# Kernel tuning notes

Hardware: AMD Instinct MI355X
Metric: run time of the kernel (lower is better)

Reference implementation:

```python
import jax, jax.numpy as jnp
import numpy as np

EPS = 1e-3  # eps in grad_pursuit_update_step


def _grad_pursuit(signal, dictionary, target_l0):
    """signal: [B, V], dictionary: [F, V] -> dense weights [B, F] (nonneg)."""
    B, V = signal.shape
    F = dictionary.shape[0]
    rows = jnp.arange(B)

    def step(weights, _):
        # residual = signal - weights @ D         [B, V]
        residual = signal - jnp.einsum('bf,fv->bv', weights, dictionary)
        # inner products with every atom          [B, F]
        inner = jnp.einsum('bv,fv->bf', residual, dictionary)
        idx = jnp.argmax(inner, axis=1)           # [B]
        selected = (weights != 0).at[rows, idx].set(True)
        grad = jnp.where(selected, inner, jnp.zeros((), signal.dtype))  # [B, F]
        c = jnp.einsum('bf,fv->bv', grad, dictionary)                   # [B, V]
        c_sq = jnp.sum(c * c, axis=-1)
        step_size = jnp.sum(c * residual, axis=-1) / jnp.maximum(c_sq, EPS)
        weights = jax.nn.relu(weights + step_size[:, None] * grad)
        return weights, None

    w0 = jnp.zeros((B, F), dtype=signal.dtype)
    weights, _ = jax.lax.scan(step, w0, None, length=target_l0)
    return weights


def _decode(indices, weights, dictionary):
    # embedding-bag sum: gather rows then weighted sum over k
    return jnp.einsum('bk,bkv->bv', weights, dictionary[indices])


def setup_inputs() -> dict:
    key = jax.random.key(0)
    k1, k2, k3, k4, k5 = jax.random.split(key, 5)
    B, D, F = 1024, 1024, 8192
    x = jax.random.normal(k1, (B, D), dtype=jnp.float32)
    y = jax.random.normal(k2, (B, D), dtype=jnp.float32)
    xs = jax.random.normal(k3, (F, D), dtype=jnp.float32)
    xs = xs / jnp.linalg.norm(xs, axis=-1, keepdims=True)  # module stores unit-norm atoms
    ys = jax.random.normal(k4, (F, D), dtype=jnp.float32)
    ys = ys / jnp.linalg.norm(jax.random.normal(k3, (F, D)), axis=-1, keepdims=True)
    mean_y = 0.1 * jax.random.normal(k5, (D,), dtype=jnp.float32)
    return {"x": x, "y": y, "xs": xs, "ys": ys, "mean_y": mean_y, "target_l0": 16}


def reference(x, y, xs, ys, mean_y, target_l0):
    # ITDA.forward with subtract_mean=False, skip_connection=False, fvu_loss=True
    dense = _grad_pursuit(x, xs, target_l0)               # [B, F]
    weights, indices = jax.lax.top_k(dense, target_l0)    # [B, k], [B, k]
    x_rec = _decode(indices, weights, xs)                  # [B, V]
    y_rec = _decode(indices, weights, ys)                  # [B, V]
    l2 = jnp.sum((y - y_rec) ** 2, axis=-1)                # [B]
    total_var = jnp.mean(jnp.sum((y - mean_y) ** 2, axis=-1))
    losses = l2 / total_var
    return weights, indices, x_rec, y_rec, losses
```

## Files before the change

### kernel.cpp

```cpp
#include <hip/hip_runtime.h>
#include <cstdint>
#include <cstddef>

#define B_N 1024
#define V_N 1024
#define F_N 8192
#define NSEL 16
#define NITER 16
#define EPSV 1e-3f
#define WINF 0.008f
#define CANDMAX 64
#define NTILE 64

#define BM 64
#define BN 128
#define BK 32
#define NBN (F_N / BN)

typedef __attribute__((ext_vector_type(4))) float f32x4;
typedef __attribute__((ext_vector_type(8))) short bf16x8;
typedef unsigned short u16;

#define GLDS16(g, l) __builtin_amdgcn_global_load_lds((__attribute__((address_space(1))) void*)(g), (__attribute__((address_space(3))) void*)(l), 16, 0, 0)

__device__ __forceinline__ u16 f2bf(float f) {
  unsigned u = __float_as_uint(f);
  return (u16)((u + 0x7FFFu + ((u >> 16) & 1u)) >> 16);
}

__device__ __forceinline__ float block_sum256(float v, float* sbuf) {
#pragma unroll
  for (int o = 32; o > 0; o >>= 1) v += __shfl_down(v, o, 64);
  int lane = threadIdx.x & 63, wid = threadIdx.x >> 6;
  if (lane == 0) sbuf[wid] = v;
  __syncthreads();
  float r = sbuf[0] + sbuf[1] + sbuf[2] + sbuf[3];
  __syncthreads();
  return r;
}

__device__ __forceinline__ float block_max256(float v, float* sbuf) {
#pragma unroll
  for (int o = 32; o > 0; o >>= 1) v = fmaxf(v, __shfl_down(v, o, 64));
  int lane = threadIdx.x & 63, wid = threadIdx.x >> 6;
  if (lane == 0) sbuf[wid] = v;
  __syncthreads();
  float r = fmaxf(fmaxf(sbuf[0], sbuf[1]), fmaxf(sbuf[2], sbuf[3]));
  __syncthreads();
  return r;
}

__device__ __forceinline__ float seq_dot(const float* __restrict__ xrow,
                                         const float* __restrict__ sr) {
  float acc = 0.f;
  for (int k = 0; k < V_N; k += 4) {
    float4 xv = *(const float4*)(xrow + k);
    acc = __builtin_fmaf(xv.x, sr[k + 0], acc);
    acc = __builtin_fmaf(xv.y, sr[k + 1], acc);
    acc = __builtin_fmaf(xv.z, sr[k + 2], acc);
    acc = __builtin_fmaf(xv.w, sr[k + 3], acc);
  }
  return acc;
}

__global__ __launch_bounds__(256) void rowvar_kernel(const float* __restrict__ y,
                                                     const float* __restrict__ mean_y,
                                                     float* __restrict__ rowvar,
                                                     int* __restrict__ act_cnt) {
  int b = blockIdx.x, t = threadIdx.x;
  __shared__ float sred[4];
  float4 yv = *(const float4*)(y + (size_t)b * V_N + t * 4);
  float4 mv = *(const float4*)(mean_y + t * 4);
  float dx = yv.x - mv.x, dy = yv.y - mv.y, dz = yv.z - mv.z, dw = yv.w - mv.w;
  float p = dx * dx + dy * dy + dz * dz + dw * dw;
  float s = block_sum256(p, sred);
  if (t == 0) { rowvar[b] = s; act_cnt[b] = 0; }
}

__global__ __launch_bounds__(256) void reduce_var_kernel(const float* __restrict__ rowvar,
                                                         float* __restrict__ totvar) {
  __shared__ float sred[4];
  int t = threadIdx.x;
  float p = 0.f;
#pragma unroll
  for (int i = 0; i < 4; i++) p += rowvar[t * 4 + i];
  float s = block_sum256(p, sred);
  if (t == 0) totvar[0] = s / (float)B_N;
}

__global__ __launch_bounds__(256) void xh_kernel(const float* __restrict__ xs,
                                                 u16* __restrict__ Xh) {
  int b = blockIdx.x, t = threadIdx.x;
  float4 v = *(const float4*)(xs + (size_t)b * V_N + t * 4);
  u16* o = Xh + (size_t)b * V_N + t * 4;
  o[0] = f2bf(v.x); o[1] = f2bf(v.y); o[2] = f2bf(v.z); o[3] = f2bf(v.w);
}

__global__ __launch_bounds__(256) void init_kernel(const float* __restrict__ x,
                                                   float* __restrict__ R,
                                                   u16* __restrict__ Rh,
                                                   float* __restrict__ rn2) {
  int b = blockIdx.x, t = threadIdx.x;
  __shared__ float sred[4];
  float4 v = *(const float4*)(x + (size_t)b * V_N + t * 4);
  *(float4*)(R + (size_t)b * V_N + t * 4) = v;
  u16* o = Rh + (size_t)b * V_N + t * 4;
  o[0] = f2bf(v.x); o[1] = f2bf(v.y); o[2] = f2bf(v.z); o[3] = f2bf(v.w);
  float p = v.x * v.x + v.y * v.y + v.z * v.z + v.w * v.w;
  float s = block_sum256(p, sred);
  if (t == 0) rn2[b] = s;
}

__global__ __launch_bounds__(256) void gemm_scan_kernel(const u16* __restrict__ Rh,
                                                        const u16* __restrict__ Xh,
                                                        float* __restrict__ inner,
                                                        float* __restrict__ pval) {
  __shared__ u16 As[128 * 32];
  __shared__ u16 Bs[128 * 32];
  __shared__ float srmax[128][2];
  const int tid = threadIdx.x;
  const int w = tid >> 6, l = tid & 63;
  const int bn = blockIdx.x, bm = blockIdx.y;
  const int wr = w >> 1, wc = w & 1;
  const int lr = l & 15, lg = l >> 4;

  f32x4 acc[4][4];
#pragma unroll
  for (int m = 0; m < 4; m++)
#pragma unroll
    for (int n = 0; n < 4; n++) acc[m][n] = (f32x4){0.f, 0.f, 0.f, 0.f};

  const u16* Ab = Rh + (size_t)bm * 128 * V_N;
  const u16* Bb = Xh + (size_t)bn * 128 * V_N;
  const int srow = w * 16 + (l >> 2);
  const int scol = (l & 3) * 8;

  for (int k0 = 0; k0 < V_N; k0 += 32) {
#pragma unroll
    for (int i = 0; i < 2; i++) {
      GLDS16(Ab + (size_t)(i * 64 + srow) * V_N + k0 + scol, As + i * 2048 + w * 512);
      GLDS16(Bb + (size_t)(i * 64 + srow) * V_N + k0 + scol, Bs + i * 2048 + w * 512);
    }
    __syncthreads();
    bf16x8 af[4], bfr[4];
#pragma unroll
    for (int m = 0; m < 4; m++) af[m] = *(const bf16x8*)&As[(wr * 64 + m * 16 + lr) * 32 + lg * 8];
#pragma unroll
    for (int n = 0; n < 4; n++) bfr[n] = *(const bf16x8*)&Bs[(wc * 64 + n * 16 + lr) * 32 + lg * 8];
#pragma unroll
    for (int m = 0; m < 4; m++)
#pragma unroll
      for (int n = 0; n < 4; n++)
        acc[m][n] = __builtin_amdgcn_mfma_f32_16x16x32_bf16(af[m], bfr[n], acc[m][n], 0, 0, 0);
    __syncthreads();
  }

#pragma unroll
  for (int m = 0; m < 4; m++) {
    int gm = bm * 128 + wr * 64 + m * 16 + lg * 4;
#pragma unroll
    for (int j = 0; j < 4; j++) {
      float pm = acc[m][0][j];
#pragma unroll
      for (int n = 1; n < 4; n++) pm = fmaxf(pm, acc[m][n][j]);
#pragma unroll
      for (int n = 0; n < 4; n++) {
        int gn = bn * 128 + wc * 64 + n * 16 + lr;
        inner[(size_t)(gm + j) * F_N + gn] = acc[m][n][j];
      }
#pragma unroll
      for (int mk = 1; mk < 16; mk <<= 1) pm = fmaxf(pm, __shfl_xor(pm, mk, 64));
      if (lr == 0) srmax[wr * 64 + m * 16 + lg * 4 + j][wc] = pm;
    }
  }
  __syncthreads();
  if (tid < 128) {
    float v = fmaxf(srmax[tid][0], srmax[tid][1]);
    pval[(size_t)(bm * 128 + tid) * NTILE + bn] = v;
  }
}

__global__ __launch_bounds__(256) void scan_update_kernel(const float* __restrict__ x,
                                                          const float* __restrict__ xs,
                                                          const float* __restrict__ inner,
                                                          const float* __restrict__ pval,
                                                          float* __restrict__ rn2,
                                                          int* __restrict__ act_ids,
                                                          float* __restrict__ act_w,
                                                          int* __restrict__ act_cnt,
                                                          float* __restrict__ R,
                                                          u16* __restrict__ Rh) {
  int b = blockIdx.x, t = threadIdx.x;
  __shared__ float sr[V_N];
  __shared__ float spv[NTILE];
  __shared__ int   shot[NTILE];
  __shared__ int   snhot;
  __shared__ float sred[4];
  __shared__ float smax[4];
  __shared__ int   scand[CANDMAX];
  __shared__ float scval[CANDMAX];
  __shared__ float sfv[256];
  __shared__ int   sfi[256];
  __shared__ int   scnt_c;
  __shared__ int   sbii;
  __shared__ float sg[NSEL + 2];
  __shared__ float sw[NSEL + 2];
  __shared__ int   sids[NSEL + 2];
  __shared__ int   ssel[NSEL + 2];
  __shared__ int   scnt;

  float4 rv = *(const float4*)(R + (size_t)b * V_N + t * 4);
  *(float4*)&sr[t * 4] = rv;
  if (t < NTILE) spv[t] = pval[(size_t)b * NTILE + t];
  if (t == 0) { scnt_c = 0; snhot = 0; }
  __syncthreads();

  float M = block_max256(spv[t & (NTILE - 1)], smax);
  float win = WINF * sqrtf(rn2[b]);
  float thr = M - win;

  if (t < NTILE && spv[t] >= thr) { int p = atomicAdd(&snhot, 1); shot[p] = t; }
  __syncthreads();
  int nh = snhot;

  const float* irow = inner + (size_t)b * F_N;
  for (int h = 0; h < nh; h++) {
    int tt = shot[h];
    if (t < 128) {
      float v = irow[tt * 128 + t];
      if (v >= thr) { int p = atomicAdd(&scnt_c, 1); if (p < CANDMAX) scand[p] = tt * 128 + t; }
    }
  }
  __syncthreads();
  int total = scnt_c;
  int nc = total < CANDMAX ? total : CANDMAX;

  if (total > CANDMAX) {
    float bv = -1e30f; int bi = 0x7fffffff;
    for (int f = t; f < F_N; f += 256) {
      float acc = seq_dot(xs + (size_t)f * V_N, sr);
      if (acc > bv) { bv = acc; bi = f; }
    }
    sfv[t] = bv; sfi[t] = bi;
    __syncthreads();
    if (t == 0) {
      float bbv = sfv[0]; int bbi = sfi[0];
      for (int c = 1; c < 256; c++) {
        float v = sfv[c]; int id = sfi[c];
        if (v > bbv || (v == bbv && id < bbi)) { bbv = v; bbi = id; }
      }
      sbii = bbi;
    }
  } else if (nc == 1) {
    if (t == 0) sbii = scand[0];
  } else {
    if (t < nc) scval[t] = seq_dot(xs + (size_t)scand[t] * V_N, sr);
    __syncthreads();
    if (t == 0) {
      float bv = scval[0]; int bi = scand[0];
      for (int c = 1; c < nc; c++) {
        float v = scval[c]; int id = scand[c];
        if (v > bv || (v == bv && id < bi)) { bv = v; bi = id; }
      }
      sbii = bi;
    }
  }
  __syncthreads();

  if (t == 0) {
    int bi = sbii;
    int cnt = act_cnt[b];
    for (int j = 0; j < cnt; j++) { sids[j] = act_ids[b * NSEL + j]; sw[j] = act_w[b * NSEL + j]; }
    int pos = -1;
    for (int j = 0; j < cnt; j++) if (sids[j] == bi) pos = j;
    if (pos < 0) { pos = cnt; sids[cnt] = bi; sw[cnt] = 0.f; cnt++; }
    for (int j = 0; j < cnt; j++) ssel[j] = (sw[j] != 0.f) || (j == pos) ? 1 : 0;
    scnt = cnt;
  }
  __syncthreads();
  int cnt = scnt;

  float4 rl = *(const float4*)&sr[t * 4];
  float4 xv[NSEL + 1];
#pragma unroll
  for (int j = 0; j < NSEL + 1; j++) {
    if (j < cnt) {
      if (ssel[j]) {
        xv[j] = *(const float4*)(xs + (size_t)sids[j] * V_N + t * 4);
        float p = xv[j].x * rl.x + xv[j].y * rl.y + xv[j].z * rl.z + xv[j].w * rl.w;
        float s = block_sum256(p, sred);
        if (t == 0) sg[j] = s;
      } else if (t == 0) sg[j] = 0.f;
    }
  }
  __syncthreads();

  float4 cv = {0.f, 0.f, 0.f, 0.f};
#pragma unroll
  for (int j = 0; j < NSEL + 1; j++) {
    if (j < cnt) {
      if (ssel[j]) {
        float g = sg[j];
        cv.x += g * xv[j].x; cv.y += g * xv[j].y; cv.z += g * xv[j].z; cv.w += g * xv[j].w;
      }
    }
  }
  float pcsq = cv.x * cv.x + cv.y * cv.y + cv.z * cv.z + cv.w * cv.w;
  float pcr  = cv.x * rl.x + cv.y * rl.y + cv.z * rl.z + cv.w * rl.w;
  float csq = block_sum256(pcsq, sred);
  float cr  = block_sum256(pcr, sred);

  if (t == 0) {
    float step = cr / fmaxf(csq, EPSV);
    for (int j = 0; j < cnt; j++)
      if (ssel[j]) sw[j] = fmaxf(sw[j] + step * sg[j], 0.f);
    for (int j = 0; j < cnt; j++) {
      act_ids[b * NSEL + j] = sids[j];
      act_w[b * NSEL + j] = sw[j];
    }
    act_cnt[b] = cnt;
  }
  __syncthreads();

  float4 r = *(const float4*)(x + (size_t)b * V_N + t * 4);
#pragma unroll
  for (int j = 0; j < NSEL + 1; j++) {
    if (j < cnt) {
      float wv = sw[j];
      if (wv != 0.f) {
        r.x -= wv * xv[j].x; r.y -= wv * xv[j].y; r.z -= wv * xv[j].z; r.w -= wv * xv[j].w;
      }
    }
  }
  *(float4*)(R + (size_t)b * V_N + t * 4) = r;
  u16* o = Rh + (size_t)b * V_N + t * 4;
  o[0] = f2bf(r.x); o[1] = f2bf(r.y); o[2] = f2bf(r.z); o[3] = f2bf(r.w);
  float p2 = r.x * r.x + r.y * r.y + r.z * r.z + r.w * r.w;
  float s2 = block_sum256(p2, sred);
  if (t == 0) rn2[b] = s2;
}

__global__ __launch_bounds__(256) void residual_kernel(const float* __restrict__ x,
                                                       const float* __restrict__ xs,
                                                       const int* __restrict__ act_ids,
                                                       const float* __restrict__ act_w,
                                                       const int* __restrict__ act_cnt,
                                                       float* __restrict__ R) {
  int b = blockIdx.x, t = threadIdx.x;
  float4 r = *(const float4*)(x + (size_t)b * V_N + t * 4);
  int cnt = act_cnt[b];
  for (int j = 0; j < cnt; j++) {
    float w = act_w[b * NSEL + j];
    if (w != 0.f) {
      const float* xr = xs + (size_t)act_ids[b * NSEL + j] * V_N;
      float4 xv = *(const float4*)(xr + t * 4);
      r.x -= w * xv.x; r.y -= w * xv.y; r.z -= w * xv.z; r.w -= w * xv.w;
    }
  }
  *(float4*)(R + (size_t)b * V_N + t * 4) = r;
}

__global__ __launch_bounds__(256) void gemm_argmax_kernel(const float* __restrict__ R,
                                                          const float* __restrict__ xs,
                                                          float* __restrict__ pval,
                                                          int* __restrict__ pidx) {
  __shared__ float sA[BK * 68];
  __shared__ float sB[BK * 132];
  __shared__ float sMv[64 * 33];
  __shared__ int   sMi[64 * 33];

  int tid = threadIdx.x;
  int bn = blockIdx.x, bm = blockIdx.y;
  float acc[8][4];
#pragma unroll
  for (int i = 0; i < 8; i++)
#pragma unroll
    for (int j = 0; j < 4; j++) acc[i][j] = 0.f;

  int r0 = (tid >> 5) << 3;
  int n0 = (tid & 31) << 2;
  const float* Rbase = R + (size_t)(bm * BM) * V_N;
  const float* Xbase = xs + (size_t)(bn * BN) * V_N;

  for (int k0 = 0; k0 < V_N; k0 += BK) {
    {
      int m = tid >> 2, kf = (tid & 3) * 4;
      float4 v = *(const float4*)(Rbase + (size_t)m * V_N + k0 + kf);
      sA[(kf + 0) * 68 + m] = v.x; sA[(kf + 1) * 68 + m] = v.y;
      sA[(kf + 2) * 68 + m] = v.z; sA[(kf + 3) * 68 + m] = v.w;
      float4 v2 = *(const float4*)(Rbase + (size_t)m * V_N + k0 + kf + 16);
      sA[(kf + 16) * 68 + m] = v2.x; sA[(kf + 17) * 68 + m] = v2.y;
      sA[(kf + 18) * 68 + m] = v2.z; sA[(kf + 19) * 68 + m] = v2.w;
    }
    {
      int nn = tid >> 3, kf = (tid & 7) * 4;
#pragma unroll
      for (int i = 0; i < 4; i++) {
        int n = nn + i * 32;
        float4 v = *(const float4*)(Xbase + (size_t)n * V_N + k0 + kf);
        sB[(kf + 0) * 132 + n] = v.x; sB[(kf + 1) * 132 + n] = v.y;
        sB[(kf + 2) * 132 + n] = v.z; sB[(kf + 3) * 132 + n] = v.w;
      }
    }
    __syncthreads();
#pragma unroll
    for (int k = 0; k < BK; k++) {
      float4 aL = *(float4*)&sA[k * 68 + r0];
      float4 aH = *(float4*)&sA[k * 68 + r0 + 4];
      float4 bv = *(float4*)&sB[k * 132 + n0];
      float a[8] = {aL.x, aL.y, aL.z, aL.w, aH.x, aH.y, aH.z, aH.w};
      float bb[4] = {bv.x, bv.y, bv.z, bv.w};
#pragma unroll
      for (int i = 0; i < 8; i++)
#pragma unroll
        for (int j = 0; j < 4; j++) acc[i][j] += a[i] * bb[j];
    }
    __syncthreads();
  }

#pragma unroll
  for (int i = 0; i < 8; i++) {
    float bvv = acc[i][0]; int bj = 0;
#pragma unroll
    for (int j = 1; j < 4; j++)
      if (acc[i][j] > bvv) { bvv = acc[i][j]; bj = j; }
    sMv[(r0 + i) * 33 + (tid & 31)] = bvv;
    sMi[(r0 + i) * 33 + (tid & 31)] = bn * BN + n0 + bj;
  }
  __syncthreads();
  if (tid < 64) {
    float bvv = sMv[tid * 33]; int bi = sMi[tid * 33];
    for (int c = 1; c < 32; c++) {
      float v = sMv[tid * 33 + c];
      if (v > bvv) { bvv = v; bi = sMi[tid * 33 + c]; }
    }
    pval[(size_t)(bm * BM + tid) * NBN + bn] = bvv;
    pidx[(size_t)(bm * BM + tid) * NBN + bn] = bi;
  }
}

__global__ __launch_bounds__(256) void combine_update_kernel(const float* __restrict__ R,
                                                             const float* __restrict__ xs,
                                                             const float* __restrict__ pval,
                                                             const int* __restrict__ pidx,
                                                             int* __restrict__ act_ids,
                                                             float* __restrict__ act_w,
                                                             int* __restrict__ act_cnt) {
  int b = blockIdx.x, t = threadIdx.x;
  __shared__ float sr[V_N];
  __shared__ float sred[4];
  __shared__ float sg[NSEL + 1];
  __shared__ float sw[NSEL + 1];
  __shared__ int   sids[NSEL + 1];
  __shared__ int   ssel[NSEL + 1];
  __shared__ int   scnt;

  float4 rv = *(const float4*)(R + (size_t)b * V_N + t * 4);
  *(float4*)&sr[t * 4] = rv;

  if (t == 0) {
    const float* pv = pval + (size_t)b * NBN;
    const int* pi = pidx + (size_t)b * NBN;
    float bv = pv[0]; int bi = pi[0];
    for (int c = 1; c < NBN; c++) {
      float v = pv[c];
      if (v > bv) { bv = v; bi = pi[c]; }
    }
    int cnt = act_cnt[b];
    for (int j = 0; j < cnt; j++) { sids[j] = act_ids[b * NSEL + j]; sw[j] = act_w[b * NSEL + j]; }
    int pos = -1;
    for (int j = 0; j < cnt; j++) if (sids[j] == bi) pos = j;
    if (pos < 0) { pos = cnt; sids[cnt] = bi; sw[cnt] = 0.f; cnt++; }
    for (int j = 0; j < cnt; j++) ssel[j] = (sw[j] != 0.f) || (j == pos) ? 1 : 0;
    scnt = cnt;
  }
  __syncthreads();
  int cnt = scnt;

  for (int j = 0; j < cnt; j++) {
    if (!ssel[j]) { if (t == 0) sg[j] = 0.f; continue; }
    const float* xr = xs + (size_t)sids[j] * V_N;
    float4 xv = *(const float4*)(xr + t * 4);
    float4 rl = *(const float4*)&sr[t * 4];
    float p = xv.x * rl.x + xv.y * rl.y + xv.z * rl.z + xv.w * rl.w;
    float s = block_sum256(p, sred);
    if (t == 0) sg[j] = s;
  }
  __syncthreads();

  float4 cv = {0.f, 0.f, 0.f, 0.f};
  for (int j = 0; j < cnt; j++) {
    if (ssel[j]) {
      float g = sg[j];
      const float* xr = xs + (size_t)sids[j] * V_N;
      float4 xv = *(const float4*)(xr + t * 4);
      cv.x += g * xv.x; cv.y += g * xv.y; cv.z += g * xv.z; cv.w += g * xv.w;
    }
  }
  float4 rl = *(const float4*)&sr[t * 4];
  float pcsq = cv.x * cv.x + cv.y * cv.y + cv.z * cv.z + cv.w * cv.w;
  float pcr  = cv.x * rl.x + cv.y * rl.y + cv.z * rl.z + cv.w * rl.w;
  float csq = block_sum256(pcsq, sred);
  float cr  = block_sum256(pcr, sred);

  if (t == 0) {
    float step = cr / fmaxf(csq, EPSV);
    for (int j = 0; j < cnt; j++)
      if (ssel[j]) sw[j] = fmaxf(sw[j] + step * sg[j], 0.f);
    for (int j = 0; j < cnt; j++) {
      act_ids[b * NSEL + j] = sids[j];
      act_w[b * NSEL + j] = sw[j];
    }
    act_cnt[b] = cnt;
  }
}

__global__ __launch_bounds__(256) void topk_kernel(const int* __restrict__ act_ids,
                                                   const float* __restrict__ act_w,
                                                   const int* __restrict__ act_cnt,
                                                   float* __restrict__ out_w,
                                                   float* __restrict__ out_i) {
  int b = blockIdx.x * blockDim.x + threadIdx.x;
  if (b >= B_N) return;
  int cnt = act_cnt[b];
  int ids[NSEL]; float w[NSEL]; int m = 0;
  for (int j = 0; j < cnt; j++) {
    float wv = act_w[b * NSEL + j];
    if (wv > 0.f) { ids[m] = act_ids[b * NSEL + j]; w[m] = wv; m++; }
  }
  for (int i = 1; i < m; i++) {
    float wv = w[i]; int id = ids[i]; int j = i - 1;
    while (j >= 0 && (w[j] < wv || (w[j] == wv && ids[j] > id))) {
      w[j + 1] = w[j]; ids[j + 1] = ids[j]; j--;
    }
    w[j + 1] = wv; ids[j + 1] = id;
  }
  int nf = 0;
  for (int s = m; s < NSEL; s++) {
    for (;;) {
      bool used = false;
      for (int j = 0; j < m; j++) if (ids[j] == nf) used = true;
      if (!used) break;
      nf++;
    }
    ids[s] = nf; w[s] = 0.f; nf++;
  }
  for (int s = 0; s < NSEL; s++) {
    out_w[b * NSEL + s] = w[s];
    out_i[b * NSEL + s] = (float)ids[s];
  }
}

__global__ __launch_bounds__(256) void decode_kernel(const float* __restrict__ y,
                                                     const float* __restrict__ xs,
                                                     const float* __restrict__ ys,
                                                     const float* __restrict__ out_w,
                                                     const float* __restrict__ out_i,
                                                     const float* __restrict__ totvar,
                                                     float* __restrict__ x_rec,
                                                     float* __restrict__ y_rec,
                                                     float* __restrict__ losses) {
  int b = blockIdx.x, t = threadIdx.x;
  __shared__ float swv[NSEL];
  __shared__ int sid[NSEL];
  __shared__ float sred[4];
  if (t < NSEL) { swv[t] = out_w[b * NSEL + t]; sid[t] = (int)out_i[b * NSEL + t]; }
  __syncthreads();
  float4 xr = {0.f, 0.f, 0.f, 0.f}, yr = {0.f, 0.f, 0.f, 0.f};
  for (int s = 0; s < NSEL; s++) {
    float wv = swv[s];
    if (wv != 0.f) {
      const float* xrow = xs + (size_t)sid[s] * V_N;
      const float* yrow = ys + (size_t)sid[s] * V_N;
      float4 a = *(const float4*)(xrow + t * 4);
      float4 c = *(const float4*)(yrow + t * 4);
      xr.x += wv * a.x; xr.y += wv * a.y; xr.z += wv * a.z; xr.w += wv * a.w;
      yr.x += wv * c.x; yr.y += wv * c.y; yr.z += wv * c.z; yr.w += wv * c.w;
    }
  }
  *(float4*)(x_rec + (size_t)b * V_N + t * 4) = xr;
  *(float4*)(y_rec + (size_t)b * V_N + t * 4) = yr;
  float4 yv = *(const float4*)(y + (size_t)b * V_N + t * 4);
  float dx = yv.x - yr.x, dy = yv.y - yr.y, dz = yv.z - yr.z, dw = yv.w - yr.w;
  float p = dx * dx + dy * dy + dz * dz + dw * dw;
  float l2 = block_sum256(p, sred);
  if (t == 0) losses[b] = l2 / totvar[0];
}

extern "C" void kernel_launch(void* const* d_in, const int* in_sizes, int n_in,
                              void* d_out, int out_size, void* d_ws, size_t ws_size,
                              hipStream_t stream) {
  const float* x      = (const float*)d_in[0];
  const float* y      = (const float*)d_in[1];
  const float* xs     = (const float*)d_in[2];
  const float* ys     = (const float*)d_in[3];
  const float* mean_y = (const float*)d_in[4];
  (void)in_sizes; (void)n_in; (void)out_size;

  float* out    = (float*)d_out;
  float* out_w  = out;
  float* out_i  = out + 16384;
  float* out_xr = out + 32768;
  float* out_yr = out + 32768 + 1048576;
  float* out_ls = out + 32768 + 2097152;

  float* ws = (float*)d_ws;

  const size_t FAST_NEED = (size_t)14257153 * 4;

  if (ws_size >= FAST_NEED) {
    float* R     = ws;
    float* inner = ws + 1048576;
    u16*   Rh    = (u16*)(ws + 9437184);
    u16*   Xh    = (u16*)(ws + 9961472);
    float* rn2   = ws + 14155776;
    int*   aid   = (int*)(ws + 14156800);
    float* aw    = ws + 14173184;
    int*   acn   = (int*)(ws + 14189568);
    float* rv    = ws + 14190592;
    float* tv    = ws + 14191616;
    float* pval  = ws + 14191617;

    rowvar_kernel<<<B_N, 256, 0, stream>>>(y, mean_y, rv, acn);
    reduce_var_kernel<<<1, 256, 0, stream>>>(rv, tv);
    xh_kernel<<<F_N, 256, 0, stream>>>(xs, Xh);
    init_kernel<<<B_N, 256, 0, stream>>>(x, R, Rh, rn2);

    for (int it = 0; it < NITER; it++) {
      gemm_scan_kernel<<<dim3(F_N / 128, B_N / 128), 256, 0, stream>>>(Rh, Xh, inner, pval);
      scan_update_kernel<<<B_N, 256, 0, stream>>>(x, xs, inner, pval, rn2, aid, aw, acn, R, Rh);
    }

    topk_kernel<<<(B_N + 255) / 256, 256, 0, stream>>>(aid, aw, acn, out_w, out_i);
    decode_kernel<<<B_N, 256, 0, stream>>>(y, xs, ys, out_w, out_i, tv, out_xr, out_yr, out_ls);
  } else {
    float* R    = ws;
    float* pval = ws + 1048576;
    int*   pidx = (int*)(ws + 1114112);
    int*   aid  = (int*)(ws + 1179648);
    float* aw   = ws + 1196032;
    int*   acn  = (int*)(ws + 1212416);
    float* rv   = ws + 1213440;
    float* tv   = ws + 1214464;

    rowvar_kernel<<<B_N, 256, 0, stream>>>(y, mean_y, rv, acn);
    reduce_var_kernel<<<1, 256, 0, stream>>>(rv, tv);

    for (int it = 0; it < NITER; it++) {
      residual_kernel<<<B_N, 256, 0, stream>>>(x, xs, aid, aw, acn, R);
      gemm_argmax_kernel<<<dim3(NBN, B_N / BM), 256, 0, stream>>>(R, xs, pval, pidx);
      combine_update_kernel<<<B_N, 256, 0, stream>>>(R, xs, pval, pidx, aid, aw, acn);
    }

    topk_kernel<<<(B_N + 255) / 256, 256, 0, stream>>>(aid, aw, acn, out_w, out_i);
    decode_kernel<<<B_N, 256, 0, stream>>>(y, xs, ys, out_w, out_i, tv, out_xr, out_yr, out_ls);
  }
}
```

Baseline: 1.147 ms.

## Store inner products as bf16, swizzle GEMM blocks, batch per-atom reductions

The GEMM now writes the [B,F] inner-product matrix as bf16 instead of fp32, halving that write and its later read. It also remaps block indices so consecutive blocks share tiles for better L2 reuse. The update kernel loads all selected atoms up front and replaces per-atom block reductions, each with two barriers, with wave-level partial sums combined after a single barrier. It also reuses the x row loaded at the start. The candidate window is widened to offset the precision lost by storing bf16, at the cost of more candidates to rescan.

```diff
diff --git a/kernel.cpp b/kernel.cpp
--- a/kernel.cpp
+++ b/kernel.cpp
@@ -8,7 +8,7 @@
 #define NSEL 16
 #define NITER 16
 #define EPSV 1e-3f
-#define WINF 0.008f
+#define WINF 0.014f
 #define CANDMAX 64
 #define NTILE 64
 
@@ -27,6 +27,9 @@
   unsigned u = __float_as_uint(f);
   return (u16)((u + 0x7FFFu + ((u >> 16) & 1u)) >> 16);
 }
+__device__ __forceinline__ float bf2f(u16 h) {
+  return __uint_as_float(((unsigned)h) << 16);
+}
 
 __device__ __forceinline__ float block_sum256(float v, float* sbuf) {
 #pragma unroll
@@ -48,6 +51,12 @@
   float r = fmaxf(fmaxf(sbuf[0], sbuf[1]), fmaxf(sbuf[2], sbuf[3]));
   __syncthreads();
   return r;
+}
+
+__device__ __forceinline__ float wave_tree64(float v) {
+#pragma unroll
+  for (int o = 32; o > 0; o >>= 1) v += __shfl_down(v, o, 64);
+  return v;
 }
 
 __device__ __forceinline__ float seq_dot(const float* __restrict__ xrow,
@@ -113,14 +122,16 @@
 
 __global__ __launch_bounds__(256) void gemm_scan_kernel(const u16* __restrict__ Rh,
                                                         const u16* __restrict__ Xh,
-                                                        float* __restrict__ inner,
+                                                        u16* __restrict__ innerH,
                                                         float* __restrict__ pval) {
   __shared__ u16 As[128 * 32];
   __shared__ u16 Bs[128 * 32];
   __shared__ float srmax[128][2];
   const int tid = threadIdx.x;
   const int w = tid >> 6, l = tid & 63;
-  const int bn = blockIdx.x, bm = blockIdx.y;
+  const int flat = blockIdx.y * 64 + blockIdx.x;
+  const int swz = (flat & 7) * 64 + (flat >> 3);
+  const int bn = swz & 63, bm = swz >> 6;
   const int wr = w >> 1, wc = w & 1;
   const int lr = l & 15, lg = l >> 4;
 
@@ -166,7 +177,7 @@
 #pragma unroll
       for (int n = 0; n < 4; n++) {
         int gn = bn * 128 + wc * 64 + n * 16 + lr;
-        inner[(size_t)(gm + j) * F_N + gn] = acc[m][n][j];
+        innerH[(size_t)(gm + j) * F_N + gn] = f2bf(acc[m][n][j]);
       }
 #pragma unroll
       for (int mk = 1; mk < 16; mk <<= 1) pm = fmaxf(pm, __shfl_xor(pm, mk, 64));
@@ -182,7 +193,7 @@
 
 __global__ __launch_bounds__(256) void scan_update_kernel(const float* __restrict__ x,
                                                           const float* __restrict__ xs,
-                                                          const float* __restrict__ inner,
+                                                          const u16* __restrict__ innerH,
                                                           const float* __restrict__ pval,
                                                           float* __restrict__ rn2,
                                                           int* __restrict__ act_ids,
@@ -203,13 +214,18 @@
   __shared__ int   sfi[256];
   __shared__ int   scnt_c;
   __shared__ int   sbii;
+  __shared__ float sgp[NSEL + 2][4];
+  __shared__ float scsqp[4], scrp[4];
   __shared__ float sg[NSEL + 2];
   __shared__ float sw[NSEL + 2];
   __shared__ int   sids[NSEL + 2];
   __shared__ int   ssel[NSEL + 2];
   __shared__ int   scnt;
 
+  const int lane = t & 63, wid = t >> 6;
+
   float4 rv = *(const float4*)(R + (size_t)b * V_N + t * 4);
+  float4 xrow = *(const float4*)(x + (size_t)b * V_N + t * 4);
   *(float4*)&sr[t * 4] = rv;
   if (t < NTILE) spv[t] = pval[(size_t)b * NTILE + t];
   if (t == 0) { scnt_c = 0; snhot = 0; }
@@ -223,11 +239,11 @@
   __syncthreads();
   int nh = snhot;
 
-  const float* irow = inner + (size_t)b * F_N;
+  const u16* irow = innerH + (size_t)b * F_N;
   for (int h = 0; h < nh; h++) {
     int tt = shot[h];
     if (t < 128) {
-      float v = irow[tt * 128 + t];
+      float v = bf2f(irow[tt * 128 + t]);
       if (v >= thr) { int p = atomicAdd(&scnt_c, 1); if (p < CANDMAX) scand[p] = tt * 128 + t; }
     }
   }
@@ -283,16 +299,24 @@
   float4 rl = *(const float4*)&sr[t * 4];
   float4 xv[NSEL + 1];
 #pragma unroll
+  for (int j = 0; j < NSEL + 1; j++)
+    if (j < cnt && ssel[j])
+      xv[j] = *(const float4*)(xs + (size_t)sids[j] * V_N + t * 4);
+
+#pragma unroll
   for (int j = 0; j < NSEL + 1; j++) {
-    if (j < cnt) {
-      if (ssel[j]) {
-        xv[j] = *(const float4*)(xs + (size_t)sids[j] * V_N + t * 4);
-        float p = xv[j].x * rl.x + xv[j].y * rl.y + xv[j].z * rl.z + xv[j].w * rl.w;
-        float s = block_sum256(p, sred);
-        if (t == 0) sg[j] = s;
-      } else if (t == 0) sg[j] = 0.f;
-    }
-  }
+    if (j < cnt && ssel[j]) {
+      float p = xv[j].x * rl.x + xv[j].y * rl.y + xv[j].z * rl.z + xv[j].w * rl.w;
+      float s = wave_tree64(p);
+      if (lane == 0) sgp[j][wid] = s;
+    }
+  }
+  if (t == 0) {
+    for (int j = 0; j < cnt; j++)
+      if (!ssel[j]) sg[j] = 0.f;
+  }
+  __syncthreads();
+  if (t < cnt && ssel[t]) sg[t] = sgp[t][0] + sgp[t][1] + sgp[t][2] + sgp[t][3];
   __syncthreads();
 
   float4 cv = {0.f, 0.f, 0.f, 0.f};
@@ -307,10 +331,16 @@
   }
   float pcsq = cv.x * cv.x + cv.y * cv.y + cv.z * cv.z + cv.w * cv.w;
   float pcr  = cv.x * rl.x + cv.y * rl.y + cv.z * rl.z + cv.w * rl.w;
-  float csq = block_sum256(pcsq, sred);
-  float cr  = block_sum256(pcr, sred);
+  {
+    float s1 = wave_tree64(pcsq);
+    float s2 = wave_tree64(pcr);
+    if (lane == 0) { scsqp[wid] = s1; scrp[wid] = s2; }
+  }
+  __syncthreads();
 
   if (t == 0) {
+    float csq = scsqp[0] + scsqp[1] + scsqp[2] + scsqp[3];
+    float cr  = scrp[0] + scrp[1] + scrp[2] + scrp[3];
     float step = cr / fmaxf(csq, EPSV);
     for (int j = 0; j < cnt; j++)
       if (ssel[j]) sw[j] = fmaxf(sw[j] + step * sg[j], 0.f);
@@ -322,7 +352,7 @@
   }
   __syncthreads();
 
-  float4 r = *(const float4*)(x + (size_t)b * V_N + t * 4);
+  float4 r = xrow;
 #pragma unroll
   for (int j = 0; j < NSEL + 1; j++) {
     if (j < cnt) {
@@ -606,20 +636,20 @@
 
   float* ws = (float*)d_ws;
 
-  const size_t FAST_NEED = (size_t)14257153 * 4;
+  const size_t FAST_NEED = (size_t)10062852 * 4;
 
   if (ws_size >= FAST_NEED) {
-    float* R     = ws;
-    float* inner = ws + 1048576;
-    u16*   Rh    = (u16*)(ws + 9437184);
-    u16*   Xh    = (u16*)(ws + 9961472);
-    float* rn2   = ws + 14155776;
-    int*   aid   = (int*)(ws + 14156800);
-    float* aw    = ws + 14173184;
-    int*   acn   = (int*)(ws + 14189568);
-    float* rv    = ws + 14190592;
-    float* tv    = ws + 14191616;
-    float* pval  = ws + 14191617;
+    float* R      = ws;
+    u16*   innerH = (u16*)(ws + 1048576);
+    u16*   Rh     = (u16*)(ws + 5242880);
+    u16*   Xh     = (u16*)(ws + 5767168);
+    float* rn2    = ws + 9961472;
+    int*   aid    = (int*)(ws + 9962496);
+    float* aw     = ws + 9978880;
+    int*   acn    = (int*)(ws + 9995264);
+    float* rv     = ws + 9996288;
+    float* tv     = ws + 9997312;
+    float* pval   = ws + 9997316;
 
     rowvar_kernel<<<B_N, 256, 0, stream>>>(y, mean_y, rv, acn);
     reduce_var_kernel<<<1, 256, 0, stream>>>(rv, tv);
@@ -627,8 +657,8 @@
     init_kernel<<<B_N, 256, 0, stream>>>(x, R, Rh, rn2);
 
     for (int it = 0; it < NITER; it++) {
-      gemm_scan_kernel<<<dim3(F_N / 128, B_N / 128), 256, 0, stream>>>(Rh, Xh, inner, pval);
-      scan_update_kernel<<<B_N, 256, 0, stream>>>(x, xs, inner, pval, rn2, aid, aw, acn, R, Rh);
+      gemm_scan_kernel<<<dim3(F_N / 128, B_N / 128), 256, 0, stream>>>(Rh, Xh, innerH, pval);
+      scan_update_kernel<<<B_N, 256, 0, stream>>>(x, xs, innerH, pval, rn2, aid, aw, acn, R, Rh);
     }
 
     topk_kernel<<<(B_N + 255) / 256, 256, 0, stream>>>(aid, aw, acn, out_w, out_i);
```

Result: slower. 3.086 ms (+169.0%).

## Overlap active-atom gradient dots with candidate argmax across waves

Applied to the files above, without the earlier changes.

Inside scan_update_kernel, waves 1-3 now compute the gradient inner products for the already-active atoms with per-wave shuffle reductions. Wave 0 meanwhile scores the candidates to find the argmax. Only the newly selected atom's dot product is computed afterwards. This replaces the serial chain of block-wide reductions, each needing two barriers, and drops the 17-entry register array of atom rows by reloading atom rows from global/cache in the later loops. The cost is extra global reloads of the atom rows, and the candidate scoring now runs on a single wave instead of the whole block.

```diff
diff --git a/kernel.cpp b/kernel.cpp
--- a/kernel.cpp
+++ b/kernel.cpp
@@ -50,6 +50,12 @@
   return r;
 }
 
+__device__ __forceinline__ float wave_tree64(float v) {
+#pragma unroll
+  for (int o = 32; o > 0; o >>= 1) v += __shfl_down(v, o, 64);
+  return v;
+}
+
 __device__ __forceinline__ float seq_dot(const float* __restrict__ xrow,
                                          const float* __restrict__ sr) {
   float acc = 0.f;
@@ -61,6 +67,21 @@
     acc = __builtin_fmaf(xv.w, sr[k + 3], acc);
   }
   return acc;
+}
+
+__device__ __forceinline__ void wave_g(const float* __restrict__ xr,
+                                       const float* __restrict__ sr,
+                                       int lane, float* __restrict__ out) {
+  float part[4];
+#pragma unroll
+  for (int vw = 0; vw < 4; vw++) {
+    int vt = vw * 64 + lane;
+    float4 xvv = *(const float4*)(xr + vt * 4);
+    float4 rl4 = *(const float4*)&sr[vt * 4];
+    float p = xvv.x * rl4.x + xvv.y * rl4.y + xvv.z * rl4.z + xvv.w * rl4.w;
+    part[vw] = wave_tree64(p);
+  }
+  if (lane == 0) *out = part[0] + part[1] + part[2] + part[3];
 }
 
 __global__ __launch_bounds__(256) void rowvar_kernel(const float* __restrict__ y,
@@ -191,6 +212,7 @@
                                                           float* __restrict__ R,
                                                           u16* __restrict__ Rh) {
   int b = blockIdx.x, t = threadIdx.x;
+  const int lane = t & 63, wid = t >> 6;
   __shared__ float sr[V_N];
   __shared__ float spv[NTILE];
   __shared__ int   shot[NTILE];
@@ -207,12 +229,16 @@
   __shared__ float sw[NSEL + 2];
   __shared__ int   sids[NSEL + 2];
   __shared__ int   ssel[NSEL + 2];
-  __shared__ int   scnt;
+  __shared__ int   scnt, scnt0, sjnew;
 
   float4 rv = *(const float4*)(R + (size_t)b * V_N + t * 4);
   *(float4*)&sr[t * 4] = rv;
   if (t < NTILE) spv[t] = pval[(size_t)b * NTILE + t];
-  if (t == 0) { scnt_c = 0; snhot = 0; }
+  if (t == 0) {
+    scnt_c = 0; snhot = 0;
+    int c0 = act_cnt[b]; scnt0 = c0;
+    for (int j = 0; j < c0; j++) { sids[j] = act_ids[b * NSEL + j]; sw[j] = act_w[b * NSEL + j]; }
+  }
   __syncthreads();
 
   float M = block_max256(spv[t & (NTILE - 1)], smax);
@@ -222,7 +248,6 @@
   if (t < NTILE && spv[t] >= thr) { int p = atomicAdd(&snhot, 1); shot[p] = t; }
   __syncthreads();
   int nh = snhot;
-
   const float* irow = inner + (size_t)b * F_N;
   for (int h = 0; h < nh; h++) {
     int tt = shot[h];
@@ -234,6 +259,29 @@
   __syncthreads();
   int total = scnt_c;
   int nc = total < CANDMAX ? total : CANDMAX;
+  int cnt0 = scnt0;
+
+  if (wid >= 1) {
+    for (int j = wid - 1; j < cnt0; j += 3) {
+      if (sw[j] != 0.f)
+        wave_g(xs + (size_t)sids[j] * V_N, sr, lane, &sg[j]);
+    }
+  } else if (total <= CANDMAX) {
+    if (nc == 1) {
+      if (lane == 0) sbii = scand[0];
+    } else {
+      if (lane < nc) scval[lane] = seq_dot(xs + (size_t)scand[lane] * V_N, sr);
+      if (lane == 0) {
+        float bv = scval[0]; int bi = scand[0];
+        for (int c = 1; c < nc; c++) {
+          float v = scval[c]; int id = scand[c];
+          if (v > bv || (v == bv && id < bi)) { bv = v; bi = id; }
+        }
+        sbii = bi;
+      }
+    }
+  }
+  __syncthreads();
 
   if (total > CANDMAX) {
     float bv = -1e30f; int bi = 0x7fffffff;
@@ -251,58 +299,35 @@
       }
       sbii = bbi;
     }
-  } else if (nc == 1) {
-    if (t == 0) sbii = scand[0];
-  } else {
-    if (t < nc) scval[t] = seq_dot(xs + (size_t)scand[t] * V_N, sr);
     __syncthreads();
-    if (t == 0) {
-      float bv = scval[0]; int bi = scand[0];
-      for (int c = 1; c < nc; c++) {
-        float v = scval[c]; int id = scand[c];
-        if (v > bv || (v == bv && id < bi)) { bv = v; bi = id; }
-      }
-      sbii = bi;
-    }
-  }
-  __syncthreads();
+  }
 
   if (t == 0) {
     int bi = sbii;
-    int cnt = act_cnt[b];
-    for (int j = 0; j < cnt; j++) { sids[j] = act_ids[b * NSEL + j]; sw[j] = act_w[b * NSEL + j]; }
+    int cnt = cnt0;
     int pos = -1;
     for (int j = 0; j < cnt; j++) if (sids[j] == bi) pos = j;
     if (pos < 0) { pos = cnt; sids[cnt] = bi; sw[cnt] = 0.f; cnt++; }
     for (int j = 0; j < cnt; j++) ssel[j] = (sw[j] != 0.f) || (j == pos) ? 1 : 0;
+    for (int j = 0; j < cnt; j++) if (!ssel[j]) sg[j] = 0.f;
+    sjnew = (sw[pos] == 0.f) ? pos : -1;
     scnt = cnt;
   }
   __syncthreads();
   int cnt = scnt;
 
+  int jnew = sjnew;
+  if (jnew >= 0 && wid == 0)
+    wave_g(xs + (size_t)sids[jnew] * V_N, sr, lane, &sg[jnew]);
+  __syncthreads();
+
   float4 rl = *(const float4*)&sr[t * 4];
-  float4 xv[NSEL + 1];
-#pragma unroll
-  for (int j = 0; j < NSEL + 1; j++) {
-    if (j < cnt) {
-      if (ssel[j]) {
-        xv[j] = *(const float4*)(xs + (size_t)sids[j] * V_N + t * 4);
-        float p = xv[j].x * rl.x + xv[j].y * rl.y + xv[j].z * rl.z + xv[j].w * rl.w;
-        float s = block_sum256(p, sred);
-        if (t == 0) sg[j] = s;
-      } else if (t == 0) sg[j] = 0.f;
-    }
-  }
-  __syncthreads();
-
   float4 cv = {0.f, 0.f, 0.f, 0.f};
-#pragma unroll
-  for (int j = 0; j < NSEL + 1; j++) {
-    if (j < cnt) {
-      if (ssel[j]) {
-        float g = sg[j];
-        cv.x += g * xv[j].x; cv.y += g * xv[j].y; cv.z += g * xv[j].z; cv.w += g * xv[j].w;
-      }
+  for (int j = 0; j < cnt; j++) {
+    if (ssel[j]) {
+      float g = sg[j];
+      float4 xvv = *(const float4*)(xs + (size_t)sids[j] * V_N + t * 4);
+      cv.x += g * xvv.x; cv.y += g * xvv.y; cv.z += g * xvv.z; cv.w += g * xvv.w;
     }
   }
   float pcsq = cv.x * cv.x + cv.y * cv.y + cv.z * cv.z + cv.w * cv.w;
@@ -323,13 +348,11 @@
   __syncthreads();
 
   float4 r = *(const float4*)(x + (size_t)b * V_N + t * 4);
-#pragma unroll
-  for (int j = 0; j < NSEL + 1; j++) {
-    if (j < cnt) {
-      float wv = sw[j];
-      if (wv != 0.f) {
-        r.x -= wv * xv[j].x; r.y -= wv * xv[j].y; r.z -= wv * xv[j].z; r.w -= wv * xv[j].w;
-      }
+  for (int j = 0; j < cnt; j++) {
+    float wv = sw[j];
+    if (wv != 0.f) {
+      float4 xvv = *(const float4*)(xs + (size_t)sids[j] * V_N + t * 4);
+      r.x -= wv * xvv.x; r.y -= wv * xvv.y; r.z -= wv * xvv.z; r.w -= wv * xvv.w;
     }
   }
   *(float4*)(R + (size_t)b * V_N + t * 4) = r;
```

After: 1.152 ms. No clear change (+0.4%).
